# Kernel tuning notes

Hardware: AMD Instinct MI355X
Metric: run time of the kernel (lower is better)

The kernel has to match this reference:

```python
import jax, jax.numpy as jnp
import numpy as np

G = 1024   # number of glimpses
P = 1024   # points per glimpse
N = G * P  # total points


def _pool(pos, batch, start, size):
    """voxel_mean_pool index computation: unique (batch, voxel) cells."""
    vox = np.floor((pos - start) / size).astype(np.int64)
    vox -= vox.min(axis=0)
    dims = vox.max(axis=0) + 1
    key = ((batch * dims[0] + vox[:, 0]) * dims[1] + vox[:, 1]) * dims[2] + vox[:, 2]
    uniq, first, inv = np.unique(key, return_index=True, return_inverse=True)
    return inv.astype(np.int64), batch[first].astype(np.int64), int(uniq.shape[0])


def setup_inputs() -> dict:
    rng = np.random.default_rng(0)
    pos = rng.uniform(-1.0, 1.0, (N, 3)).astype(np.float32)
    rgb = rng.random((N, 1)).astype(np.float32)
    batch = np.repeat(np.arange(G, dtype=np.int64), P)
    # min_pos gets a random negative offset (noise) in the torch code
    min_pos = pos.min(axis=0) - rng.random(3).astype(np.float32)
    # level-1 voxel pooling (size 0.25)
    cluster1, batch1, M1 = _pool(pos, batch, min_pos, 0.25)
    cnt1 = np.bincount(cluster1, minlength=M1).astype(np.float32)[:, None]
    ps1 = np.zeros((M1, 3), np.float32)
    np.add.at(ps1, cluster1, pos)
    ps1 /= cnt1
    # level-2 voxel pooling (size 0.5) on voxel centers
    cluster2, batch2, M2 = _pool(ps1, batch1, min_pos, 0.5)

    def lin(fi, fo):
        return (rng.standard_normal((fi, fo)).astype(np.float32) / np.sqrt(fi))

    d = dict(
        rgb=jnp.asarray(rgb), pos=jnp.asarray(pos),
        glimpse_center=jnp.asarray(rng.standard_normal((G, 3)).astype(np.float32)),
        W1l=jnp.asarray(lin(1 + 3, 16)), b1l=jnp.zeros(16, jnp.float32),
        W1g=jnp.asarray(lin(16, 32)), b1g=jnp.zeros(32, jnp.float32),
        W2l=jnp.asarray(lin(32 + 3, 64)), b2l=jnp.zeros(64, jnp.float32),
        W2g=jnp.asarray(lin(64, 128)), b2g=jnp.zeros(128, jnp.float32),
        W3l=jnp.asarray(lin(128 + 3, 128)), b3l=jnp.zeros(128, jnp.float32),
        W3g=jnp.asarray(lin(128, 256)), b3g=jnp.zeros(256, jnp.float32),
        Wlin=jnp.asarray(lin(256, 256)), blin=jnp.zeros(256, jnp.float32),
        eps=jnp.asarray(rng.standard_normal((G, 128)).astype(np.float32)),
        glimpse_index=jnp.asarray(batch),
        cluster1=jnp.asarray(cluster1), cluster2=jnp.asarray(cluster2),
        batch2=jnp.asarray(batch2),
        num_voxels1=M1, num_voxels2=M2,
    )
    return d


def _seg_mean(x, seg, m):
    s = jax.ops.segment_sum(x, seg, num_segments=m)
    c = jax.ops.segment_sum(jnp.ones((x.shape[0], 1), x.dtype), seg, num_segments=m)
    return s / jnp.maximum(c, 1.0)


def _point_conv(x_in, pos_in, pos_out, out_index, Wl, bl, Wg, bg, m_out):
    # gather: relative position of each input point to its output (voxel) center
    rel = pos_in - pos_out[out_index]                      # [E,3]
    msg = jax.nn.relu(jnp.concatenate([x_in, rel], 1) @ Wl + bl)  # [E,c_mid]
    agg = jax.ops.segment_max(msg, out_index, num_segments=m_out)  # [M,c_mid]
    return agg @ Wg + bg


def reference(rgb, pos, glimpse_center, W1l, b1l, W1g, b1g, W2l, b2l, W2g, b2g,
              W3l, b3l, W3g, b3g, Wlin, blin, eps, glimpse_index,
              cluster1, cluster2, batch2, num_voxels1, num_voxels2):
    M1, M2 = num_voxels1, num_voxels2
    Gn = glimpse_center.shape[0]
    # stage 1: voxel mean pool (0.25) + PointConv 1->16->32
    ps1 = _seg_mean(pos, cluster1, M1)                     # [M1,3]
    f1 = jax.nn.celu(_point_conv(rgb, pos, ps1, cluster1, W1l, b1l, W1g, b1g, M1))
    # stage 2: voxel mean pool (0.5) + PointConv 32->64->128
    ps2 = _seg_mean(ps1, cluster2, M2)                     # [M2,3]
    f2 = jax.nn.celu(_point_conv(f1, ps1, ps2, cluster2, W2l, b2l, W2g, b2g, M2))
    # stage 3: pool everything to the glimpse center (pos_out = zeros)
    pos_out = jnp.zeros_like(glimpse_center)
    f3 = jax.nn.celu(_point_conv(f2, ps2, pos_out, batch2, W3l, b3l, W3g, b3g, Gn))
    # head: Linear(256,256), split into mu/sigma, reparameterized sample
    out = f3 @ Wlin + blin                                 # [G,256]
    mu, s = jnp.split(out, 2, axis=1)
    sigma = jax.nn.softplus(s)
    z = mu + sigma * eps                                   # [G,128]
    z_what, z_mask = jnp.split(z, 2, axis=1)
    return z_what, z_mask, mu, sigma, f3
```

## Files before the change

### kernel.cpp

```cpp
#include <hip/hip_runtime.h>
#include <math.h>

#define N1CAP 736
#define N2CAP 192
#define S3 132

__device__ __forceinline__ float celu1(float x){ return x > 0.f ? x : (expf(x) - 1.f); }
__device__ __forceinline__ float softplus1(float x){ return fmaxf(x, 0.f) + log1pf(expf(-fabsf(x))); }
__device__ __forceinline__ void atomicMaxNonneg(float* p, float v){
    atomicMax((int*)p, __float_as_int(v));
}

__global__ __launch_bounds__(256) void kA(const float* __restrict__ rgb,
                                          const float* __restrict__ pos,
                                          const int* __restrict__ cl1,
                                          const float* __restrict__ W1l,
                                          const float* __restrict__ b1l,
                                          float* __restrict__ ps1,
                                          float* __restrict__ agg1,
                                          float* __restrict__ cnt1,
                                          int* __restrict__ seg1, int P){
    __shared__ float sp[3*1024];
    __shared__ float srgb[1024];
    __shared__ int   ci[1024];
    __shared__ int   cnt[N1CAP];
    __shared__ int   start[N1CAP+1];
    __shared__ int   cur[N1CAP];
    __shared__ unsigned short pidx[1024];
    __shared__ float wsh[64], bsh[16];
    __shared__ int   red[2];
    __shared__ int   wsum[4];
    const int g = blockIdx.x, tid = threadIdx.x;
    const int base = g * P;
    const bool pfit = (P <= 1024);

    if (tid == 0){ red[0] = 0x7fffffff; red[1] = -1; }
    if (tid < 64) wsh[tid] = W1l[tid];
    if (tid < 16) bsh[tid] = b1l[tid];
    __syncthreads();
    int mn = 0x7fffffff, mx = -1;
    for (int i = tid; i < P; i += 256){
        int c = cl1[base+i];
        if (pfit) ci[i] = c;
        mn = min(mn,c); mx = max(mx,c);
    }
    atomicMin(&red[0], mn); atomicMax(&red[1], mx);
    __syncthreads();
    const int s1 = red[0];
    const int n1 = red[1] - red[0] + 1;
    const bool fast = pfit && (n1 <= N1CAP);

    if (fast){
        for (int t = tid; t < 3*P; t += 256) sp[t] = pos[(size_t)base*3 + t];
        for (int t = tid; t < P;   t += 256) srgb[t] = rgb[base + t];
        for (int l = tid; l < n1;  l += 256) cnt[l] = 0;
        __syncthreads();
        for (int i = tid; i < P; i += 256) atomicAdd(&cnt[ci[i] - s1], 1);
        __syncthreads();
        {
            int b3 = tid*3;
            int a0 = (b3   < n1) ? cnt[b3]   : 0;
            int a1 = (b3+1 < n1) ? cnt[b3+1] : 0;
            int a2 = (b3+2 < n1) ? cnt[b3+2] : 0;
            int s = a0+a1+a2;
            int lane = tid & 63, wv = tid >> 6;
            int ps = s;
            #pragma unroll
            for (int d = 1; d < 64; d <<= 1){
                int t2 = __shfl_up(ps, d, 64);
                if (lane >= d) ps += t2;
            }
            if (lane == 63) wsum[wv] = ps;
            __syncthreads();
            int woff = 0;
            #pragma unroll
            for (int w = 0; w < 4; ++w) woff += (w < wv) ? wsum[w] : 0;
            int excl = woff + ps - s;
            if (b3   < n1){ start[b3]   = excl;       cur[b3]   = excl; }
            if (b3+1 < n1){ start[b3+1] = excl+a0;    cur[b3+1] = excl+a0; }
            if (b3+2 < n1){ start[b3+2] = excl+a0+a1; cur[b3+2] = excl+a0+a1; }
            if (tid == 0) start[n1] = P;
        }
        __syncthreads();
        for (int i = tid; i < P; i += 256){
            int slot = atomicAdd(&cur[ci[i] - s1], 1);
            pidx[slot] = (unsigned short)i;
        }
        __syncthreads();
        for (int l = tid; l < n1; l += 256){
            int s0 = start[l], e0 = start[l+1];
            float sxv=0.f, syv=0.f, szv=0.f;
            for (int k = s0; k < e0; ++k){
                int i = pidx[k];
                sxv += sp[3*i+0]; syv += sp[3*i+1]; szv += sp[3*i+2];
            }
            float ic = 1.0f / (float)max(e0 - s0, 1);
            float mxp = sxv*ic, myp = syv*ic, mzp = szv*ic;
            ps1[(size_t)(s1+l)*3+0] = mxp;
            ps1[(size_t)(s1+l)*3+1] = myp;
            ps1[(size_t)(s1+l)*3+2] = mzp;
            float acc[16];
            #pragma unroll
            for (int j = 0; j < 16; ++j) acc[j] = 0.f;
            for (int k = s0; k < e0; ++k){
                int i = pidx[k];
                float in0 = srgb[i];
                float r0 = sp[3*i+0] - mxp;
                float r1 = sp[3*i+1] - myp;
                float r2 = sp[3*i+2] - mzp;
                #pragma unroll
                for (int j = 0; j < 16; ++j){
                    float v = bsh[j] + in0*wsh[j] + r0*wsh[16+j] + r1*wsh[32+j] + r2*wsh[48+j];
                    acc[j] = fmaxf(acc[j], fmaxf(v, 0.f));
                }
            }
            float4* dst = (float4*)&agg1[(size_t)(s1+l)*16];
            dst[0] = make_float4(acc[0], acc[1], acc[2], acc[3]);
            dst[1] = make_float4(acc[4], acc[5], acc[6], acc[7]);
            dst[2] = make_float4(acc[8], acc[9], acc[10], acc[11]);
            dst[3] = make_float4(acc[12], acc[13], acc[14], acc[15]);
        }
    } else {
        for (int t = tid; t < n1;    t += 256) cnt1[s1+t] = 0.f;
        for (int t = tid; t < n1*3;  t += 256) ps1[(size_t)s1*3+t] = 0.f;
        for (int t = tid; t < n1*16; t += 256) agg1[(size_t)s1*16+t] = 0.f;
        __syncthreads();
        for (int i = tid; i < P; i += 256){
            int idx = base + i; int c = cl1[idx];
            atomicAdd(&ps1[3*c+0], pos[3*idx+0]);
            atomicAdd(&ps1[3*c+1], pos[3*idx+1]);
            atomicAdd(&ps1[3*c+2], pos[3*idx+2]);
            atomicAdd(&cnt1[c], 1.0f);
        }
        __syncthreads();
        for (int l = tid; l < n1; l += 256){
            float ic = 1.0f / fmaxf(cnt1[s1+l], 1.0f);
            ps1[(size_t)(s1+l)*3+0] *= ic; ps1[(size_t)(s1+l)*3+1] *= ic; ps1[(size_t)(s1+l)*3+2] *= ic;
        }
        __syncthreads();
        for (int i = tid; i < P; i += 256){
            int idx = base + i; int c = cl1[idx];
            float in0 = rgb[idx];
            float r0 = pos[3*idx+0] - ps1[3*c+0];
            float r1 = pos[3*idx+1] - ps1[3*c+1];
            float r2 = pos[3*idx+2] - ps1[3*c+2];
            #pragma unroll
            for (int j = 0; j < 16; ++j){
                float v = b1l[j] + in0*W1l[j] + r0*W1l[16+j] + r1*W1l[32+j] + r2*W1l[48+j];
                atomicMaxNonneg(&agg1[(size_t)c*16+j], fmaxf(v, 0.0f));
            }
        }
    }
    if (tid == 0){ seg1[2*g] = s1; seg1[2*g+1] = n1; }
}

__global__ __launch_bounds__(256) void kB(const float* __restrict__ ps1,
                                          const float* __restrict__ agg1,
                                          const int* __restrict__ cl2,
                                          const float* __restrict__ W1g,
                                          const float* __restrict__ b1g,
                                          const float* __restrict__ W2l,
                                          const float* __restrict__ b2l,
                                          const int* __restrict__ seg1,
                                          float* __restrict__ ps2,
                                          float* __restrict__ agg2,
                                          float* __restrict__ cnt2,
                                          int* __restrict__ seg2){
    __shared__ float sx[N2CAP], sy[N2CAP], sz[N2CAP], sc[N2CAP];
    __shared__ float sagg[N2CAP*64];
    __shared__ int red[2];
    const int g = blockIdx.x, tid = threadIdx.x;
    const int s1 = seg1[2*g], n1 = seg1[2*g+1], e1 = s1 + n1;

    if (tid == 0){ red[0] = 0x7fffffff; red[1] = -1; }
    __syncthreads();
    int mn = 0x7fffffff, mx = -1;
    for (int m = s1 + tid; m < e1; m += 256){ int c = cl2[m]; mn = min(mn,c); mx = max(mx,c); }
    atomicMin(&red[0], mn); atomicMax(&red[1], mx);
    __syncthreads();
    const int s2 = red[0];
    const int n2 = red[1] - red[0] + 1;
    const bool fast = (n2 <= N2CAP);

    if (fast){
        for (int l = tid; l < n2; l += 256){ sx[l]=0.f; sy[l]=0.f; sz[l]=0.f; sc[l]=0.f; }
        for (int t = tid; t < n2*64; t += 256) sagg[t] = 0.f;
        __syncthreads();
        for (int m = s1 + tid; m < e1; m += 256){
            int c = cl2[m] - s2;
            atomicAdd(&sx[c], ps1[3*m+0]);
            atomicAdd(&sy[c], ps1[3*m+1]);
            atomicAdd(&sz[c], ps1[3*m+2]);
            atomicAdd(&sc[c], 1.0f);
        }
        __syncthreads();
        for (int l = tid; l < n2; l += 256){
            float ic = 1.0f / sc[l];
            sx[l] *= ic; sy[l] *= ic; sz[l] *= ic;
        }
        __syncthreads();
        for (int t = tid; t < n2*3; t += 256){
            int l = t/3, d = t - 3*l;
            ps2[(size_t)s2*3 + t] = (d==0) ? sx[l] : ((d==1) ? sy[l] : sz[l]);
        }
        for (int m = s1 + tid; m < e1; m += 256){
            float a[16];
            const float* ar = agg1 + (size_t)m*16;
            #pragma unroll
            for (int k = 0; k < 16; ++k) a[k] = ar[k];
            float in[35];
            for (int j = 0; j < 32; j += 4){
                float v0=b1g[j+0], v1=b1g[j+1], v2=b1g[j+2], v3=b1g[j+3];
                #pragma unroll
                for (int k = 0; k < 16; ++k){
                    float x = a[k];
                    const float* w = &W1g[k*32 + j];
                    v0 += x*w[0]; v1 += x*w[1]; v2 += x*w[2]; v3 += x*w[3];
                }
                in[j+0]=celu1(v0); in[j+1]=celu1(v1); in[j+2]=celu1(v2); in[j+3]=celu1(v3);
            }
            int c = cl2[m] - s2;
            in[32] = ps1[3*m+0] - sx[c];
            in[33] = ps1[3*m+1] - sy[c];
            in[34] = ps1[3*m+2] - sz[c];
            float* dst = &sagg[c*64];
            for (int j = 0; j < 64; j += 4){
                float v0=b2l[j+0], v1=b2l[j+1], v2=b2l[j+2], v3=b2l[j+3];
                #pragma unroll
                for (int k = 0; k < 35; ++k){
                    float x = in[k];
                    const float* w = &W2l[k*64 + j];
                    v0 += x*w[0]; v1 += x*w[1]; v2 += x*w[2]; v3 += x*w[3];
                }
                atomicMaxNonneg(&dst[(j+0 + c) & 63], fmaxf(v0, 0.0f));
                atomicMaxNonneg(&dst[(j+1 + c) & 63], fmaxf(v1, 0.0f));
                atomicMaxNonneg(&dst[(j+2 + c) & 63], fmaxf(v2, 0.0f));
                atomicMaxNonneg(&dst[(j+3 + c) & 63], fmaxf(v3, 0.0f));
            }
        }
        __syncthreads();
        for (int t = tid; t < n2*64; t += 256){
            int l = t >> 6, j = t & 63;
            agg2[(size_t)s2*64 + t] = sagg[l*64 + ((j + l) & 63)];
        }
    } else {
        for (int t = tid; t < n2;    t += 256) cnt2[s2+t] = 0.f;
        for (int t = tid; t < n2*3;  t += 256) ps2[(size_t)s2*3+t] = 0.f;
        for (int t = tid; t < n2*64; t += 256) agg2[(size_t)s2*64+t] = 0.f;
        __syncthreads();
        for (int m = s1 + tid; m < e1; m += 256){
            int c = cl2[m];
            atomicAdd(&ps2[3*c+0], ps1[3*m+0]);
            atomicAdd(&ps2[3*c+1], ps1[3*m+1]);
            atomicAdd(&ps2[3*c+2], ps1[3*m+2]);
            atomicAdd(&cnt2[c], 1.0f);
        }
        __syncthreads();
        for (int l = tid; l < n2; l += 256){
            float ic = 1.0f / fmaxf(cnt2[s2+l], 1.0f);
            ps2[(size_t)(s2+l)*3+0] *= ic; ps2[(size_t)(s2+l)*3+1] *= ic; ps2[(size_t)(s2+l)*3+2] *= ic;
        }
        __syncthreads();
        for (int m = s1 + tid; m < e1; m += 256){
            float a[16];
            const float* ar = agg1 + (size_t)m*16;
            #pragma unroll
            for (int k = 0; k < 16; ++k) a[k] = ar[k];
            float in[35];
            #pragma unroll
            for (int j = 0; j < 32; ++j){
                float v = b1g[j];
                #pragma unroll
                for (int k = 0; k < 16; ++k) v += a[k] * W1g[k*32+j];
                in[j] = celu1(v);
            }
            int c = cl2[m];
            in[32] = ps1[3*m+0] - ps2[3*c+0];
            in[33] = ps1[3*m+1] - ps2[3*c+1];
            in[34] = ps1[3*m+2] - ps2[3*c+2];
            for (int j = 0; j < 64; ++j){
                float v = b2l[j];
                #pragma unroll
                for (int k = 0; k < 35; ++k) v += in[k] * W2l[k*64+j];
                atomicMaxNonneg(&agg2[(size_t)c*64+j], fmaxf(v, 0.0f));
            }
        }
    }
    if (tid == 0){ seg2[2*g] = s2; seg2[2*g+1] = n2; }
}

__global__ __launch_bounds__(256) void k_f2f(const float* __restrict__ agg2,
                                             const float* __restrict__ W2g,
                                             const float* __restrict__ b2g,
                                             float* __restrict__ f2, int M2){
    __shared__ float Ws[64*128];
    __shared__ float xt[32*S3];
    const int tid = threadIdx.x;
    const int m0 = blockIdx.x * 128;
    for (int t = tid; t < 64*128; t += 256) Ws[t] = W2g[t];
    const int tr = tid & 31, tc = tid >> 5;
    float acc[4][16];
    #pragma unroll
    for (int c = 0; c < 16; ++c){
        float b = b2g[tc*16 + c];
        #pragma unroll
        for (int r = 0; r < 4; ++r) acc[r][c] = b;
    }
    for (int c0 = 0; c0 < 64; c0 += 32){
        __syncthreads();
        for (int t = tid; t < 128*8; t += 256){
            int row = t >> 3, kq = t & 7;
            int m = m0 + row;
            float4 v = (m < M2) ? *(const float4*)&agg2[(size_t)m*64 + c0 + kq*4]
                                : make_float4(0.f,0.f,0.f,0.f);
            xt[(kq*4+0)*S3 + row] = v.x;
            xt[(kq*4+1)*S3 + row] = v.y;
            xt[(kq*4+2)*S3 + row] = v.z;
            xt[(kq*4+3)*S3 + row] = v.w;
        }
        __syncthreads();
        #pragma unroll 4
        for (int kk = 0; kk < 32; ++kk){
            int k = c0 + kk;
            float4 xr = *(const float4*)&xt[kk*S3 + tr*4];
            float xv[4] = {xr.x, xr.y, xr.z, xr.w};
            float wv[16];
            #pragma unroll
            for (int q = 0; q < 4; ++q){
                float4 w = *(const float4*)&Ws[k*128 + tc*16 + q*4];
                wv[q*4+0]=w.x; wv[q*4+1]=w.y; wv[q*4+2]=w.z; wv[q*4+3]=w.w;
            }
            #pragma unroll
            for (int r = 0; r < 4; ++r)
                #pragma unroll
                for (int c = 0; c < 16; ++c) acc[r][c] += xv[r]*wv[c];
        }
    }
    #pragma unroll
    for (int r = 0; r < 4; ++r){
        int m = m0 + tr*4 + r;
        if (m < M2){
            #pragma unroll
            for (int q = 0; q < 4; ++q){
                float4 o;
                o.x = celu1(acc[r][q*4+0]); o.y = celu1(acc[r][q*4+1]);
                o.z = celu1(acc[r][q*4+2]); o.w = celu1(acc[r][q*4+3]);
                *(float4*)&f2[(size_t)m*128 + tc*16 + q*4] = o;
            }
        }
    }
}

__global__ __launch_bounds__(256) void k_msg3g(const float* __restrict__ f2,
                                               const float* __restrict__ ps2,
                                               const int* __restrict__ seg2,
                                               const float* __restrict__ W3l,
                                               const float* __restrict__ b3l,
                                               float* __restrict__ agg3, int G){
    __shared__ float Wh[131*64];
    __shared__ float xt[32*S3];
    __shared__ float shAgg[128];
    const int tid = threadIdx.x;
    const int cb = blockIdx.y * 64;
    const int g0 = blockIdx.x * 2;
    const int S  = seg2[2*g0];
    const int B  = seg2[2*g0+1];
    const int n2b = (g0 + 1 < G) ? seg2[2*g0+3] : 0;
    const int T  = B + n2b;
    for (int t = tid; t < 131*64; t += 256){
        int k = t >> 6, c = t & 63;
        Wh[t] = W3l[k*128 + cb + c];
    }
    if (tid < 128) shAgg[tid] = 0.f;
    const int tr = tid & 31, tc = tid >> 5;
    float bias[8];
    #pragma unroll
    for (int c = 0; c < 8; ++c) bias[c] = b3l[cb + tc*8 + c];

    for (int w0 = 0; w0 < T; w0 += 128){
        float acc[4][8];
        #pragma unroll
        for (int r = 0; r < 4; ++r)
            #pragma unroll
            for (int c = 0; c < 8; ++c) acc[r][c] = bias[c];
        for (int c0 = 0; c0 < 128; c0 += 32){
            __syncthreads();
            for (int t = tid; t < 128*8; t += 256){
                int row = t >> 3, kq = t & 7;
                int ridx = w0 + row;
                float4 v = (ridx < T) ? *(const float4*)&f2[(size_t)(S+ridx)*128 + c0 + kq*4]
                                      : make_float4(0.f,0.f,0.f,0.f);
                xt[(kq*4+0)*S3 + row] = v.x;
                xt[(kq*4+1)*S3 + row] = v.y;
                xt[(kq*4+2)*S3 + row] = v.z;
                xt[(kq*4+3)*S3 + row] = v.w;
            }
            __syncthreads();
            #pragma unroll 8
            for (int kk = 0; kk < 32; ++kk){
                int k = c0 + kk;
                float4 xr = *(const float4*)&xt[kk*S3 + tr*4];
                float xv[4] = {xr.x, xr.y, xr.z, xr.w};
                float4 wa = *(const float4*)&Wh[k*64 + tc*8];
                float4 wb = *(const float4*)&Wh[k*64 + tc*8 + 4];
                float wv[8] = {wa.x,wa.y,wa.z,wa.w, wb.x,wb.y,wb.z,wb.w};
                #pragma unroll
                for (int r = 0; r < 4; ++r)
                    #pragma unroll
                    for (int c = 0; c < 8; ++c) acc[r][c] += xv[r]*wv[c];
            }
        }
        #pragma unroll
        for (int kk = 0; kk < 3; ++kk){
            const float* w = &Wh[(128+kk)*64 + tc*8];
            float wv[8];
            #pragma unroll
            for (int c = 0; c < 8; ++c) wv[c] = w[c];
            #pragma unroll
            for (int r = 0; r < 4; ++r){
                int ridx = w0 + tr*4 + r;
                float x = (ridx < T) ? ps2[(size_t)(S+ridx)*3 + kk] : 0.f;
                #pragma unroll
                for (int c = 0; c < 8; ++c) acc[r][c] += x*wv[c];
            }
        }
        float mx0[8], mx1[8];
        #pragma unroll
        for (int c = 0; c < 8; ++c){ mx0[c] = 0.f; mx1[c] = 0.f; }
        bool h0 = false, h1 = false;
        #pragma unroll
        for (int r = 0; r < 4; ++r){
            int ridx = w0 + tr*4 + r;
            if (ridx < T){
                bool second = (ridx >= B);
                h0 |= !second; h1 |= second;
                #pragma unroll
                for (int c = 0; c < 8; ++c){
                    float v = fmaxf(acc[r][c], 0.f);
                    mx0[c] = fmaxf(mx0[c], second ? 0.f : v);
                    mx1[c] = fmaxf(mx1[c], second ? v : 0.f);
                }
            }
        }
        if (h0){
            #pragma unroll
            for (int c = 0; c < 8; ++c) atomicMaxNonneg(&shAgg[tc*8 + c], mx0[c]);
        }
        if (h1){
            #pragma unroll
            for (int c = 0; c < 8; ++c) atomicMaxNonneg(&shAgg[64 + tc*8 + c], mx1[c]);
        }
    }
    __syncthreads();
    if (tid < 128){
        int loc = tid >> 6, c = tid & 63;
        int g = g0 + loc;
        if (loc == 0 || n2b > 0)
            agg3[(size_t)g*128 + cb + c] = shAgg[loc*64 + c];
    }
}

__global__ __launch_bounds__(256) void k_head(const float* __restrict__ agg3,
                                              const float* __restrict__ W3g,
                                              const float* __restrict__ b3g,
                                              const float* __restrict__ Wlin,
                                              const float* __restrict__ blin,
                                              const float* __restrict__ eps,
                                              float* __restrict__ out, int G){
    __shared__ float a3[128];
    __shared__ float f3s[256];
    __shared__ float hs[256];
    int g = blockIdx.x;
    int j = threadIdx.x;
    if (j < 128) a3[j] = agg3[(size_t)g*128 + j];
    __syncthreads();

    float v = b3g[j];
    for (int k = 0; k < 128; ++k) v += a3[k] * W3g[k*256 + j];
    v = celu1(v);
    f3s[j] = v;
    const size_t o_zm = (size_t)64*G, o_mu = (size_t)128*G, o_sg = (size_t)256*G, o_f3 = (size_t)384*G;
    out[o_f3 + (size_t)g*256 + j] = v;
    __syncthreads();

    float h = blin[j];
    for (int k = 0; k < 256; ++k) h += f3s[k] * Wlin[k*256 + j];
    hs[j] = h;
    __syncthreads();

    if (j < 128){
        float mu = hs[j];
        float sg = softplus1(hs[128 + j]);
        float z = mu + sg * eps[(size_t)g*128 + j];
        out[o_mu + (size_t)g*128 + j] = mu;
        out[o_sg + (size_t)g*128 + j] = sg;
        if (j < 64) out[(size_t)g*64 + j] = z;
        else        out[o_zm + (size_t)g*64 + (j - 64)] = z;
    }
}

extern "C" void kernel_launch(void* const* d_in, const int* in_sizes, int n_in,
                              void* d_out, int out_size, void* d_ws, size_t ws_size,
                              hipStream_t stream) {
    const float* rgb  = (const float*)d_in[0];
    const float* pos  = (const float*)d_in[1];
    const float* W1l  = (const float*)d_in[3];
    const float* b1l  = (const float*)d_in[4];
    const float* W1g  = (const float*)d_in[5];
    const float* b1g  = (const float*)d_in[6];
    const float* W2l  = (const float*)d_in[7];
    const float* b2l  = (const float*)d_in[8];
    const float* W2g  = (const float*)d_in[9];
    const float* b2g  = (const float*)d_in[10];
    const float* W3l  = (const float*)d_in[11];
    const float* b3l  = (const float*)d_in[12];
    const float* W3g  = (const float*)d_in[13];
    const float* b3g  = (const float*)d_in[14];
    const float* Wlin = (const float*)d_in[15];
    const float* blin = (const float*)d_in[16];
    const float* eps  = (const float*)d_in[17];
    const int* cl1 = (const int*)d_in[19];
    const int* cl2 = (const int*)d_in[20];

    const int N  = in_sizes[19];
    const int G  = in_sizes[17] / 128;
    const int M1 = in_sizes[20];
    const int M2 = in_sizes[21];
    const int P  = N / G;

    char* ws = (char*)d_ws;
    auto al = [](size_t x){ return (x + 255) & ~(size_t)255; };
    size_t off = 0;
    float* ps1  = (float*)(ws + off); off = al(off + 12ull*M1);
    size_t uni  = ((size_t)64*M1 > (size_t)512*M2) ? (size_t)64*M1 : (size_t)512*M2;
    float* agg1 = (float*)(ws + off);
    float* f2   = (float*)(ws + off);
    off = al(off + uni);
    float* cnt1 = (float*)(ws + off); off = al(off + 4ull*M1);
    float* ps2  = (float*)(ws + off); off = al(off + 12ull*M2);
    float* agg2 = (float*)(ws + off); off = al(off + 256ull*M2);
    float* cnt2 = (float*)(ws + off); off = al(off + 4ull*M2);
    float* agg3 = (float*)(ws + off); off = al(off + 512ull*G);
    int*   seg1 = (int*)  (ws + off); off = al(off + 8ull*G);
    int*   seg2 = (int*)  (ws + off); off = al(off + 8ull*G);
    if (off > ws_size) return;

    kA<<<G, 256, 0, stream>>>(rgb, pos, cl1, W1l, b1l, ps1, agg1, cnt1, seg1, P);
    kB<<<G, 256, 0, stream>>>(ps1, agg1, cl2, W1g, b1g, W2l, b2l, seg1, ps2, agg2, cnt2, seg2);
    int gx = (M2 + 127) / 128;
    k_f2f  <<<gx, 256, 0, stream>>>(agg2, W2g, b2g, f2, M2);
    dim3 g3((G + 1) / 2, 2);
    k_msg3g<<<g3, 256, 0, stream>>>(f2, ps2, seg2, W3l, b3l, agg3, G);
    k_head <<<G, 256, 0, stream>>>(agg3, W3g, b3g, Wlin, blin, eps, (float*)d_out, G);
}
```

Baseline: 397.5 us.

## Tile kB point MLP through shared memory and pool four glimpses per msg3 block

```diff
diff --git a/kernel.cpp b/kernel.cpp
--- a/kernel.cpp
+++ b/kernel.cpp
@@ -2,7 +2,7 @@
 #include <math.h>
 
 #define N1CAP 736
-#define N2CAP 192
+#define N2CAP 160
 #define S3 132
 
 __device__ __forceinline__ float celu1(float x){ return x > 0.f ? x : (expf(x) - 1.f); }
@@ -168,7 +168,9 @@
                                           int* __restrict__ seg2){
     __shared__ float sx[N2CAP], sy[N2CAP], sz[N2CAP], sc[N2CAP];
     __shared__ float sagg[N2CAP*64];
-    __shared__ int red[2];
+    __shared__ float xt[35*S3];
+    __shared__ int   cid[128];
+    __shared__ int   red[2];
     const int g = blockIdx.x, tid = threadIdx.x;
     const int s1 = seg1[2*g], n1 = seg1[2*g+1], e1 = s1 + n1;
 
@@ -203,39 +205,93 @@
             int l = t/3, d = t - 3*l;
             ps2[(size_t)s2*3 + t] = (d==0) ? sx[l] : ((d==1) ? sy[l] : sz[l]);
         }
-        for (int m = s1 + tid; m < e1; m += 256){
-            float a[16];
-            const float* ar = agg1 + (size_t)m*16;
-            #pragma unroll
-            for (int k = 0; k < 16; ++k) a[k] = ar[k];
-            float in[35];
-            for (int j = 0; j < 32; j += 4){
-                float v0=b1g[j+0], v1=b1g[j+1], v2=b1g[j+2], v3=b1g[j+3];
-                #pragma unroll
-                for (int k = 0; k < 16; ++k){
-                    float x = a[k];
-                    const float* w = &W1g[k*32 + j];
-                    v0 += x*w[0]; v1 += x*w[1]; v2 += x*w[2]; v3 += x*w[3];
+        const int tr = tid & 31;
+        const int tcg = tid >> 5;
+        for (int t0 = 0; t0 < n1; t0 += 128){
+            int nr = min(128, n1 - t0);
+            __syncthreads();
+            for (int t = tid; t < 512; t += 256){
+                int row = t >> 2, kq = t & 3;
+                float4 v = (row < nr) ? *(const float4*)&agg1[(size_t)(s1+t0+row)*16 + kq*4]
+                                      : make_float4(0.f,0.f,0.f,0.f);
+                xt[(kq*4+0)*S3 + row] = v.x;
+                xt[(kq*4+1)*S3 + row] = v.y;
+                xt[(kq*4+2)*S3 + row] = v.z;
+                xt[(kq*4+3)*S3 + row] = v.w;
+            }
+            if (tid < 128){
+                int row = tid;
+                if (row < nr){
+                    int m = s1 + t0 + row;
+                    int c = cl2[m] - s2;
+                    cid[row] = c;
+                    xt[32*S3 + row] = ps1[3*m+0] - sx[c];
+                    xt[33*S3 + row] = ps1[3*m+1] - sy[c];
+                    xt[34*S3 + row] = ps1[3*m+2] - sz[c];
+                } else {
+                    cid[row] = -1;
+                    xt[32*S3 + row] = 0.f; xt[33*S3 + row] = 0.f; xt[34*S3 + row] = 0.f;
                 }
-                in[j+0]=celu1(v0); in[j+1]=celu1(v1); in[j+2]=celu1(v2); in[j+3]=celu1(v3);
-            }
-            int c = cl2[m] - s2;
-            in[32] = ps1[3*m+0] - sx[c];
-            in[33] = ps1[3*m+1] - sy[c];
-            in[34] = ps1[3*m+2] - sz[c];
-            float* dst = &sagg[c*64];
-            for (int j = 0; j < 64; j += 4){
-                float v0=b2l[j+0], v1=b2l[j+1], v2=b2l[j+2], v3=b2l[j+3];
-                #pragma unroll
-                for (int k = 0; k < 35; ++k){
-                    float x = in[k];
-                    const float* w = &W2l[k*64 + j];
-                    v0 += x*w[0]; v1 += x*w[1]; v2 += x*w[2]; v3 += x*w[3];
+            }
+            __syncthreads();
+            float a1[4][4];
+            #pragma unroll
+            for (int c = 0; c < 4; ++c){
+                float b = b1g[tcg*4 + c];
+                #pragma unroll
+                for (int r = 0; r < 4; ++r) a1[r][c] = b;
+            }
+            #pragma unroll
+            for (int k = 0; k < 16; ++k){
+                float4 xr = *(const float4*)&xt[k*S3 + tr*4];
+                float xv[4] = {xr.x, xr.y, xr.z, xr.w};
+                float4 w = *(const float4*)&W1g[k*32 + tcg*4];
+                float wv[4] = {w.x, w.y, w.z, w.w};
+                #pragma unroll
+                for (int r = 0; r < 4; ++r)
+                    #pragma unroll
+                    for (int c = 0; c < 4; ++c) a1[r][c] += xv[r]*wv[c];
+            }
+            __syncthreads();
+            #pragma unroll
+            for (int c = 0; c < 4; ++c){
+                float4 o;
+                o.x = celu1(a1[0][c]); o.y = celu1(a1[1][c]);
+                o.z = celu1(a1[2][c]); o.w = celu1(a1[3][c]);
+                *(float4*)&xt[(tcg*4+c)*S3 + tr*4] = o;
+            }
+            __syncthreads();
+            float acc[4][8];
+            #pragma unroll
+            for (int c = 0; c < 8; ++c){
+                float b = b2l[tcg*8 + c];
+                #pragma unroll
+                for (int r = 0; r < 4; ++r) acc[r][c] = b;
+            }
+            #pragma unroll
+            for (int k = 0; k < 35; ++k){
+                float4 xr = *(const float4*)&xt[k*S3 + tr*4];
+                float xv[4] = {xr.x, xr.y, xr.z, xr.w};
+                float4 wa = *(const float4*)&W2l[k*64 + tcg*8];
+                float4 wb = *(const float4*)&W2l[k*64 + tcg*8 + 4];
+                float wv[8] = {wa.x,wa.y,wa.z,wa.w, wb.x,wb.y,wb.z,wb.w};
+                #pragma unroll
+                for (int r = 0; r < 4; ++r)
+                    #pragma unroll
+                    for (int c = 0; c < 8; ++c) acc[r][c] += xv[r]*wv[c];
+            }
+            #pragma unroll
+            for (int r = 0; r < 4; ++r){
+                int row = tr*4 + r;
+                int c = cid[row];
+                if (c >= 0){
+                    float* dst = &sagg[c*64];
+                    #pragma unroll
+                    for (int cc = 0; cc < 8; ++cc){
+                        int ch = tcg*8 + cc;
+                        atomicMaxNonneg(&dst[(ch + c) & 63], fmaxf(acc[r][cc], 0.f));
+                    }
                 }
-                atomicMaxNonneg(&dst[(j+0 + c) & 63], fmaxf(v0, 0.0f));
-                atomicMaxNonneg(&dst[(j+1 + c) & 63], fmaxf(v1, 0.0f));
-                atomicMaxNonneg(&dst[(j+2 + c) & 63], fmaxf(v2, 0.0f));
-                atomicMaxNonneg(&dst[(j+3 + c) & 63], fmaxf(v3, 0.0f));
             }
         }
         __syncthreads();
@@ -359,19 +415,21 @@
                                                float* __restrict__ agg3, int G){
     __shared__ float Wh[131*64];
     __shared__ float xt[32*S3];
-    __shared__ float shAgg[128];
+    __shared__ float shAgg[256];
     const int tid = threadIdx.x;
     const int cb = blockIdx.y * 64;
-    const int g0 = blockIdx.x * 2;
+    const int g0 = blockIdx.x * 4;
     const int S  = seg2[2*g0];
-    const int B  = seg2[2*g0+1];
-    const int n2b = (g0 + 1 < G) ? seg2[2*g0+3] : 0;
-    const int T  = B + n2b;
+    int n0 = seg2[2*g0+1];
+    int nA = (g0+1 < G) ? seg2[2*(g0+1)+1] : 0;
+    int nB = (g0+2 < G) ? seg2[2*(g0+2)+1] : 0;
+    int nC = (g0+3 < G) ? seg2[2*(g0+3)+1] : 0;
+    const int B1 = n0, B2 = B1 + nA, B3 = B2 + nB, T = B3 + nC;
     for (int t = tid; t < 131*64; t += 256){
         int k = t >> 6, c = t & 63;
         Wh[t] = W3l[k*128 + cb + c];
     }
-    if (tid < 128) shAgg[tid] = 0.f;
+    shAgg[tid] = 0.f;
     const int tr = tid & 31, tc = tid >> 5;
     float bias[8];
     #pragma unroll
@@ -424,38 +482,39 @@
                 for (int c = 0; c < 8; ++c) acc[r][c] += x*wv[c];
             }
         }
-        float mx0[8], mx1[8];
-        #pragma unroll
-        for (int c = 0; c < 8; ++c){ mx0[c] = 0.f; mx1[c] = 0.f; }
-        bool h0 = false, h1 = false;
+        float mx[8];
+        int cur = -1;
         #pragma unroll
         for (int r = 0; r < 4; ++r){
             int ridx = w0 + tr*4 + r;
             if (ridx < T){
-                bool second = (ridx >= B);
-                h0 |= !second; h1 |= second;
-                #pragma unroll
-                for (int c = 0; c < 8; ++c){
-                    float v = fmaxf(acc[r][c], 0.f);
-                    mx0[c] = fmaxf(mx0[c], second ? 0.f : v);
-                    mx1[c] = fmaxf(mx1[c], second ? v : 0.f);
+                int loc = (ridx >= B1) + (ridx >= B2) + (ridx >= B3);
+                if (loc != cur){
+                    if (cur >= 0){
+                        #pragma unroll
+                        for (int c = 0; c < 8; ++c)
+                            atomicMaxNonneg(&shAgg[cur*64 + tc*8 + c], mx[c]);
+                    }
+                    cur = loc;
+                    #pragma unroll
+                    for (int c = 0; c < 8; ++c) mx[c] = fmaxf(acc[r][c], 0.f);
+                } else {
+                    #pragma unroll
+                    for (int c = 0; c < 8; ++c) mx[c] = fmaxf(mx[c], fmaxf(acc[r][c], 0.f));
                 }
             }
         }
-        if (h0){
-            #pragma unroll
-            for (int c = 0; c < 8; ++c) atomicMaxNonneg(&shAgg[tc*8 + c], mx0[c]);
-        }
-        if (h1){
-            #pragma unroll
-            for (int c = 0; c < 8; ++c) atomicMaxNonneg(&shAgg[64 + tc*8 + c], mx1[c]);
-        }
-    }
-    __syncthreads();
-    if (tid < 128){
+        if (cur >= 0){
+            #pragma unroll
+            for (int c = 0; c < 8; ++c)
+                atomicMaxNonneg(&shAgg[cur*64 + tc*8 + c], mx[c]);
+        }
+    }
+    __syncthreads();
+    {
         int loc = tid >> 6, c = tid & 63;
         int g = g0 + loc;
-        if (loc == 0 || n2b > 0)
+        if (g < G)
             agg3[(size_t)g*128 + cb + c] = shAgg[loc*64 + c];
     }
 }
@@ -549,7 +608,7 @@
     kB<<<G, 256, 0, stream>>>(ps1, agg1, cl2, W1g, b1g, W2l, b2l, seg1, ps2, agg2, cnt2, seg2);
     int gx = (M2 + 127) / 128;
     k_f2f  <<<gx, 256, 0, stream>>>(agg2, W2g, b2g, f2, M2);
-    dim3 g3((G + 1) / 2, 2);
+    dim3 g3((G + 3) / 4, 2);
     k_msg3g<<<g3, 256, 0, stream>>>(f2, ps2, seg2, W3l, b3l, agg3, G);
     k_head <<<G, 256, 0, stream>>>(agg3, W3g, b3g, Wlin, blin, eps, (float*)d_out, G);
 }
```

Result: slower. 606.1 us (+52.5%).
